# Performance work log

Hardware: AMD Instinct MI355X
Metric: run time of the kernel (lower is better)

## Reference

```python
import jax, jax.numpy as jnp
import numpy as np

B, H = 65536, 19


def _nbr(x):
    # 4-neighbor sum, equivalent to conv2d with cross kernel [[0,1,0],[1,0,1],[0,1,0]], padding=1
    p = jnp.pad(x, ((0, 0), (1, 1), (1, 1)))
    return p[:, :-2, 1:-1] + p[:, 2:, 1:-1] + p[:, 1:-1, :-2] + p[:, 1:-1, 2:]


def setup_inputs() -> dict:
    key = jax.random.key(0)
    k1, k2, k3 = jax.random.split(key, 3)
    # ternary board: 0 empty, 1 black, 2 white -> disjoint stone planes
    board = jax.random.randint(k1, (B, H, H), 0, 3)
    stones = jnp.stack([(board == 1), (board == 2)], axis=1).astype(jnp.float32)  # [B,2,H,H]
    current_player = jax.random.randint(k2, (B,), 0, 2, dtype=jnp.int32)
    ko_points = jax.random.randint(k3, (B, 2), 0, H, dtype=jnp.int32)  # all kos active (>=0)
    return {"stones": stones, "current_player": current_player, "ko_points": ko_points}


def reference(stones, current_player, ko_points):
    f32 = jnp.float32
    cp = current_player[:, None, None]  # [B,1,1]
    cur = jnp.where(cp == 0, stones[:, 0], stones[:, 1])  # [B,H,H] float 0/1
    opp = jnp.where(cp == 0, stones[:, 1], stones[:, 0])
    empty = 1.0 - stones[:, 0] - stones[:, 1]             # float 0/1 (planes disjoint)
    empty_b = empty > 0.5

    # legal_moves()
    legal = empty_b & (_nbr(empty) > 0)
    opp_lib = _nbr(opp)
    weak = (opp > 0.5) & (opp_lib == 1)
    adj_weak = _nbr(weak.astype(f32)) > 0
    legal = legal | (empty_b & adj_weak)
    ids = jnp.arange(stones.shape[0])
    has_ko = ko_points[:, 0] >= 0
    rr = jnp.clip(ko_points[:, 0], 0, H - 1)
    cc = jnp.clip(ko_points[:, 1], 0, H - 1)
    legal = legal.at[ids, rr, cc].set(jnp.where(has_ko, False, legal[ids, rr, cc]))

    cur_lib = _nbr(cur) * empty
    turn = jnp.broadcast_to(current_player.astype(f32)[:, None, None], (stones.shape[0], H, H))
    return jnp.stack([cur, opp, legal.astype(f32), cur_lib, turn], axis=1)  # [B,5,H,H]
```

## Files before the change

### kernel.cpp

```cpp
#include <hip/hip_runtime.h>

#define GO_H 19
#define GO_HP 21
#define NCELL (GO_H * GO_H)
#define NPAD  (GO_HP * GO_HP)

__global__ __launch_bounds__(256) void go_features_kernel(
    const float* __restrict__ stones,
    const int*   __restrict__ cur_player,
    const int*   __restrict__ ko,
    float*       __restrict__ out)
{
    __shared__ float cur_p[NPAD];
    __shared__ float opp_p[NPAD];
    __shared__ float emp_p[NPAD];
    __shared__ float weak_p[NPAD];

    const int b   = blockIdx.x;
    const int tid = threadIdx.x;
    const int cp  = cur_player[b];

    const long long ibase = (long long)b * (2 * NCELL);
    const long long obase = (long long)b * (5 * NCELL);

    for (int i = tid; i < NPAD; i += 256) {
        cur_p[i]  = 0.f;
        opp_p[i]  = 0.f;
        emp_p[i]  = 0.f;
        weak_p[i] = 0.f;
    }
    __syncthreads();

    #pragma unroll
    for (int k = 0; k < 2; ++k) {
        int c = tid + k * 256;
        if (c < NCELL) {
            float s0 = stones[ibase + c];
            float s1 = stones[ibase + NCELL + c];
            float cu = cp ? s1 : s0;
            float op = cp ? s0 : s1;
            float em = 1.0f - s0 - s1;
            int r = c / GO_H, col = c % GO_H;
            int pi = (r + 1) * GO_HP + (col + 1);
            cur_p[pi] = cu;
            opp_p[pi] = op;
            emp_p[pi] = em;
        }
    }
    __syncthreads();

    #pragma unroll
    for (int k = 0; k < 2; ++k) {
        int c = tid + k * 256;
        if (c < NCELL) {
            int r = c / GO_H, col = c % GO_H;
            int pi = (r + 1) * GO_HP + (col + 1);
            float opl = opp_p[pi - GO_HP] + opp_p[pi + GO_HP]
                      + opp_p[pi - 1]     + opp_p[pi + 1];
            weak_p[pi] = (opp_p[pi] > 0.5f && opl == 1.0f) ? 1.f : 0.f;
        }
    }
    __syncthreads();

    int kr = ko[2 * b], kc = ko[2 * b + 1];
    bool has_ko = (kr >= 0);
    int rr = min(max(kr, 0), GO_H - 1);
    int cc = min(max(kc, 0), GO_H - 1);
    int koc = rr * GO_H + cc;
    float turn = (float)cp;

    #pragma unroll
    for (int k = 0; k < 2; ++k) {
        int c = tid + k * 256;
        if (c < NCELL) {
            int r = c / GO_H, col = c % GO_H;
            int pi = (r + 1) * GO_HP + (col + 1);
            float em  = emp_p[pi];
            bool  emb = em > 0.5f;
            float ne = emp_p[pi - GO_HP] + emp_p[pi + GO_HP]
                     + emp_p[pi - 1]     + emp_p[pi + 1];
            float nw = weak_p[pi - GO_HP] + weak_p[pi + GO_HP]
                     + weak_p[pi - 1]     + weak_p[pi + 1];
            bool legal = emb && (ne > 0.f || nw > 0.f);
            if (has_ko && c == koc) legal = false;
            float nc = cur_p[pi - GO_HP] + cur_p[pi + GO_HP]
                     + cur_p[pi - 1]     + cur_p[pi + 1];

            out[obase + c]             = cur_p[pi];
            out[obase + NCELL + c]     = opp_p[pi];
            out[obase + 2 * NCELL + c] = legal ? 1.f : 0.f;
            out[obase + 3 * NCELL + c] = nc * em;
            out[obase + 4 * NCELL + c] = turn;
        }
    }
}

extern "C" void kernel_launch(void* const* d_in, const int* in_sizes, int n_in,
                              void* d_out, int out_size, void* d_ws, size_t ws_size,
                              hipStream_t stream) {
    const float* stones     = (const float*)d_in[0];
    const int*   cur_player = (const int*)d_in[1];
    const int*   ko         = (const int*)d_in[2];
    float*       out        = (float*)d_out;

    const int B = in_sizes[1];
    go_features_kernel<<<B, 256, 0, stream>>>(stones, cur_player, ko, out);
}
```

Before: 607.7 us.

## Process four boards per block with vectorized raw loads and masked stencils

Each block now handles four boards instead of one. It copies the raw stone planes into shared memory with float4 loads and computes the padding-free neighbour sums using boundary masks rather than zero-padded shared buffers. This removes the per-board padding initialisation and one barrier, and it raises thread utilisation from 361 of 512 slots to full 256-wide loops over 1444 cells. The launch assumes B is divisible by 4 and that the stone base address is 16-byte aligned. Per-cell index arithmetic grows from the div/mod and mask selects.

```diff
diff --git a/kernel.cpp b/kernel.cpp
--- a/kernel.cpp
+++ b/kernel.cpp
@@ -1,97 +1,118 @@
 #include <hip/hip_runtime.h>
 
 #define GO_H 19
-#define GO_HP 21
-#define NCELL (GO_H * GO_H)
-#define NPAD  (GO_HP * GO_HP)
+#define NCELL 361
+#define G 4
+#define NIN (G * 2 * NCELL)
+#define NC_G (G * NCELL)
 
 __global__ __launch_bounds__(256) void go_features_kernel(
     const float* __restrict__ stones,
     const int*   __restrict__ cur_player,
     const int*   __restrict__ ko,
-    float*       __restrict__ out)
+    float*       __restrict__ out,
+    int B)
 {
-    __shared__ float cur_p[NPAD];
-    __shared__ float opp_p[NPAD];
-    __shared__ float emp_p[NPAD];
-    __shared__ float weak_p[NPAD];
+    __shared__ float sarr[NIN];
+    __shared__ float weak_s[NC_G];
+    __shared__ int   cp_s[G];
+    __shared__ int   koc_s[G];
+    __shared__ int   opp_off_s[G];
 
-    const int b   = blockIdx.x;
     const int tid = threadIdx.x;
-    const int cp  = cur_player[b];
+    const int gb  = blockIdx.x * G;
 
-    const long long ibase = (long long)b * (2 * NCELL);
-    const long long obase = (long long)b * (5 * NCELL);
+    {
+        const float4* in4 = (const float4*)(stones + (size_t)gb * (2 * NCELL));
+        float4* s4 = (float4*)sarr;
+        #pragma unroll
+        for (int i = tid; i < NIN / 4; i += 256) s4[i] = in4[i];
+    }
 
-    for (int i = tid; i < NPAD; i += 256) {
-        cur_p[i]  = 0.f;
-        opp_p[i]  = 0.f;
-        emp_p[i]  = 0.f;
-        weak_p[i] = 0.f;
+    if (tid < G) {
+        int b  = gb + tid;
+        int cp = cur_player[b];
+        cp_s[tid] = cp;
+        opp_off_s[tid] = tid * (2 * NCELL) + (cp == 0 ? NCELL : 0);
+        int kr = ko[2 * b], kc = ko[2 * b + 1];
+        int rr = min(max(kr, 0), GO_H - 1);
+        int cc = min(max(kc, 0), GO_H - 1);
+        koc_s[tid] = (kr >= 0) ? (rr * GO_H + cc) : -1;
     }
     __syncthreads();
 
-    #pragma unroll
-    for (int k = 0; k < 2; ++k) {
-        int c = tid + k * 256;
-        if (c < NCELL) {
-            float s0 = stones[ibase + c];
-            float s1 = stones[ibase + NCELL + c];
-            float cu = cp ? s1 : s0;
-            float op = cp ? s0 : s1;
-            float em = 1.0f - s0 - s1;
-            int r = c / GO_H, col = c % GO_H;
-            int pi = (r + 1) * GO_HP + (col + 1);
-            cur_p[pi] = cu;
-            opp_p[pi] = op;
-            emp_p[pi] = em;
-        }
+    for (int i = tid; i < NC_G; i += 256) {
+        int g   = i / NCELL;
+        int c   = i - g * NCELL;
+        int r   = c / GO_H;
+        int col = c - r * GO_H;
+        int ob  = opp_off_s[g];
+
+        float mu = (r > 0)          ? 1.f : 0.f;
+        float md = (r < GO_H - 1)   ? 1.f : 0.f;
+        float ml = (col > 0)        ? 1.f : 0.f;
+        float mr = (col < GO_H - 1) ? 1.f : 0.f;
+        int iu = (r > 0)          ? c - GO_H : c;
+        int id = (r < GO_H - 1)   ? c + GO_H : c;
+        int il = (col > 0)        ? c - 1    : c;
+        int ir = (col < GO_H - 1) ? c + 1    : c;
+
+        float opl = sarr[ob + iu] * mu + sarr[ob + id] * md
+                  + sarr[ob + il] * ml + sarr[ob + ir] * mr;
+        float osf = sarr[ob + c];
+        weak_s[i] = (osf > 0.5f && opl == 1.0f) ? 1.f : 0.f;
     }
     __syncthreads();
 
-    #pragma unroll
-    for (int k = 0; k < 2; ++k) {
-        int c = tid + k * 256;
-        if (c < NCELL) {
-            int r = c / GO_H, col = c % GO_H;
-            int pi = (r + 1) * GO_HP + (col + 1);
-            float opl = opp_p[pi - GO_HP] + opp_p[pi + GO_HP]
-                      + opp_p[pi - 1]     + opp_p[pi + 1];
-            weak_p[pi] = (opp_p[pi] > 0.5f && opl == 1.0f) ? 1.f : 0.f;
+    for (int i = tid; i < NC_G; i += 256) {
+        int g   = i / NCELL;
+        int c   = i - g * NCELL;
+        int r   = c / GO_H;
+        int col = c - r * GO_H;
+        int base = g * (2 * NCELL);
+        int cp   = cp_s[g];
+        int wb   = g * NCELL;
+
+        float mu = (r > 0)          ? 1.f : 0.f;
+        float md = (r < GO_H - 1)   ? 1.f : 0.f;
+        float ml = (col > 0)        ? 1.f : 0.f;
+        float mr = (col < GO_H - 1) ? 1.f : 0.f;
+        int iu = (r > 0)          ? c - GO_H : c;
+        int id = (r < GO_H - 1)   ? c + GO_H : c;
+        int il = (col > 0)        ? c - 1    : c;
+        int ir = (col < GO_H - 1) ? c + 1    : c;
+
+        float s0 = sarr[base + c];
+        float s1 = sarr[base + NCELL + c];
+        float cu = cp ? s1 : s0;
+        float op = cp ? s0 : s1;
+        float em = 1.f - s0 - s1;
+
+        float ne = 0.f, ncur = 0.f;
+        {
+            float n0, n1;
+            n0 = sarr[base + iu]; n1 = sarr[base + NCELL + iu];
+            ne += (1.f - n0 - n1) * mu;  ncur += (cp ? n1 : n0) * mu;
+            n0 = sarr[base + id]; n1 = sarr[base + NCELL + id];
+            ne += (1.f - n0 - n1) * md;  ncur += (cp ? n1 : n0) * md;
+            n0 = sarr[base + il]; n1 = sarr[base + NCELL + il];
+            ne += (1.f - n0 - n1) * ml;  ncur += (cp ? n1 : n0) * ml;
+            n0 = sarr[base + ir]; n1 = sarr[base + NCELL + ir];
+            ne += (1.f - n0 - n1) * mr;  ncur += (cp ? n1 : n0) * mr;
         }
-    }
-    __syncthreads();
+        float nw = weak_s[wb + iu] * mu + weak_s[wb + id] * md
+                 + weak_s[wb + il] * ml + weak_s[wb + ir] * mr;
 
-    int kr = ko[2 * b], kc = ko[2 * b + 1];
-    bool has_ko = (kr >= 0);
-    int rr = min(max(kr, 0), GO_H - 1);
-    int cc = min(max(kc, 0), GO_H - 1);
-    int koc = rr * GO_H + cc;
-    float turn = (float)cp;
+        bool emb   = em > 0.5f;
+        bool legal = emb && (ne > 0.f || nw > 0.f);
+        if (c == koc_s[g]) legal = false;
 
-    #pragma unroll
-    for (int k = 0; k < 2; ++k) {
-        int c = tid + k * 256;
-        if (c < NCELL) {
-            int r = c / GO_H, col = c % GO_H;
-            int pi = (r + 1) * GO_HP + (col + 1);
-            float em  = emp_p[pi];
-            bool  emb = em > 0.5f;
-            float ne = emp_p[pi - GO_HP] + emp_p[pi + GO_HP]
-                     + emp_p[pi - 1]     + emp_p[pi + 1];
-            float nw = weak_p[pi - GO_HP] + weak_p[pi + GO_HP]
-                     + weak_p[pi - 1]     + weak_p[pi + 1];
-            bool legal = emb && (ne > 0.f || nw > 0.f);
-            if (has_ko && c == koc) legal = false;
-            float nc = cur_p[pi - GO_HP] + cur_p[pi + GO_HP]
-                     + cur_p[pi - 1]     + cur_p[pi + 1];
-
-            out[obase + c]             = cur_p[pi];
-            out[obase + NCELL + c]     = opp_p[pi];
-            out[obase + 2 * NCELL + c] = legal ? 1.f : 0.f;
-            out[obase + 3 * NCELL + c] = nc * em;
-            out[obase + 4 * NCELL + c] = turn;
-        }
+        size_t obase = (size_t)(gb + g) * (5 * NCELL);
+        out[obase + c]             = cu;
+        out[obase + NCELL + c]     = op;
+        out[obase + 2 * NCELL + c] = legal ? 1.f : 0.f;
+        out[obase + 3 * NCELL + c] = ncur * em;
+        out[obase + 4 * NCELL + c] = (float)cp;
     }
 }
 
@@ -104,5 +125,6 @@
     float*       out        = (float*)d_out;
 
     const int B = in_sizes[1];
-    go_features_kernel<<<B, 256, 0, stream>>>(stones, cur_player, ko, out);
+    const int nblocks = B / G;
+    go_features_kernel<<<nblocks, 256, 0, stream>>>(stones, cur_player, ko, out, B);
 }
```

Result: faster. 583.3 us (-4.0%).

## Process two boards per block with border-only zeroing and index LUT

Applied to the files above, without the earlier changes.

Each 256-thread block now handles two boards instead of one, so 722 cells are spread across three thread iterations and fewer lanes sit idle. Only the padding border of the shared tiles is zeroed, the zeroing pass and its barrier are dropped, and a shared lookup table stores the padded index so the later passes skip the divide and modulo. Player and ko data are staged in shared memory. The cost is more shared memory per block and fewer blocks, and B must be divisible by two.

```diff
diff --git a/kernel.cpp b/kernel.cpp
--- a/kernel.cpp
+++ b/kernel.cpp
@@ -1,9 +1,11 @@
 #include <hip/hip_runtime.h>
 
-#define GO_H 19
+#define GO_H  19
 #define GO_HP 21
-#define NCELL (GO_H * GO_H)
-#define NPAD  (GO_HP * GO_HP)
+#define NCELL 361
+#define NPAD  441
+#define G     2
+#define NC_G  (G * NCELL)
 
 __global__ __launch_bounds__(256) void go_features_kernel(
     const float* __restrict__ stones,
@@ -11,86 +13,104 @@
     const int*   __restrict__ ko,
     float*       __restrict__ out)
 {
-    __shared__ float cur_p[NPAD];
-    __shared__ float opp_p[NPAD];
-    __shared__ float emp_p[NPAD];
-    __shared__ float weak_p[NPAD];
+    __shared__ float cur_p[G][NPAD];
+    __shared__ float opp_p[G][NPAD];
+    __shared__ float emp_p[G][NPAD];
+    __shared__ float weak_p[G][NPAD];
+    __shared__ unsigned short lut[NCELL];
+    __shared__ int cp_s[G], koc_s[G];
 
-    const int b   = blockIdx.x;
     const int tid = threadIdx.x;
-    const int cp  = cur_player[b];
+    const int gb  = blockIdx.x * G;
 
-    const long long ibase = (long long)b * (2 * NCELL);
-    const long long obase = (long long)b * (5 * NCELL);
-
-    for (int i = tid; i < NPAD; i += 256) {
-        cur_p[i]  = 0.f;
-        opp_p[i]  = 0.f;
-        emp_p[i]  = 0.f;
-        weak_p[i] = 0.f;
-    }
-    __syncthreads();
 
     #pragma unroll
     for (int k = 0; k < 2; ++k) {
-        int c = tid + k * 256;
-        if (c < NCELL) {
-            float s0 = stones[ibase + c];
-            float s1 = stones[ibase + NCELL + c];
-            float cu = cp ? s1 : s0;
-            float op = cp ? s0 : s1;
-            float em = 1.0f - s0 - s1;
-            int r = c / GO_H, col = c % GO_H;
-            int pi = (r + 1) * GO_HP + (col + 1);
-            cur_p[pi] = cu;
-            opp_p[pi] = op;
-            emp_p[pi] = em;
+        int i = tid + k * 256;
+        if (i < NPAD) {
+            int r = i / GO_HP, col = i - r * GO_HP;
+            if (r == 0 || r == GO_HP - 1 || col == 0 || col == GO_HP - 1) {
+                #pragma unroll
+                for (int g = 0; g < G; ++g) {
+                    cur_p[g][i] = 0.f; opp_p[g][i] = 0.f;
+                    emp_p[g][i] = 0.f; weak_p[g][i] = 0.f;
+                }
+            } else {
+                lut[(r - 1) * GO_H + (col - 1)] = (unsigned short)i;
+            }
+        }
+    }
+
+    if (tid < G) {
+        int b = gb + tid;
+        cp_s[tid] = cur_player[b];
+        int kr = ko[2 * b], kc = ko[2 * b + 1];
+        int rr = min(max(kr, 0), GO_H - 1);
+        int cc = min(max(kc, 0), GO_H - 1);
+        koc_s[tid] = (kr >= 0) ? rr * GO_H + cc : -1;
+    }
+
+    {
+        int c = tid, g = 0;
+        #pragma unroll
+        for (int k = 0; k < 3; ++k) {
+            if (g < G) {
+                int   cp = cur_player[gb + g];
+                const float* bp = stones + (size_t)(gb + g) * (2 * NCELL);
+                float s0 = bp[c];
+                float s1 = bp[NCELL + c];
+                int r = c / GO_H, col = c - r * GO_H;
+                int pi = (r + 1) * GO_HP + col + 1;
+                cur_p[g][pi] = cp ? s1 : s0;
+                opp_p[g][pi] = cp ? s0 : s1;
+                emp_p[g][pi] = 1.f - s0 - s1;
+            }
+            c += 256; if (c >= NCELL) { c -= NCELL; ++g; }
         }
     }
     __syncthreads();
 
-    #pragma unroll
-    for (int k = 0; k < 2; ++k) {
-        int c = tid + k * 256;
-        if (c < NCELL) {
-            int r = c / GO_H, col = c % GO_H;
-            int pi = (r + 1) * GO_HP + (col + 1);
-            float opl = opp_p[pi - GO_HP] + opp_p[pi + GO_HP]
-                      + opp_p[pi - 1]     + opp_p[pi + 1];
-            weak_p[pi] = (opp_p[pi] > 0.5f && opl == 1.0f) ? 1.f : 0.f;
+    {
+        int c = tid, g = 0;
+        #pragma unroll
+        for (int k = 0; k < 3; ++k) {
+            if (g < G) {
+                int pi = lut[c];
+                float o = opp_p[g][pi];
+                float s = opp_p[g][pi - GO_HP] + opp_p[g][pi + GO_HP]
+                        + opp_p[g][pi - 1]     + opp_p[g][pi + 1];
+                weak_p[g][pi] = (o > 0.5f && s == 1.0f) ? 1.f : 0.f;
+            }
+            c += 256; if (c >= NCELL) { c -= NCELL; ++g; }
         }
     }
     __syncthreads();
 
-    int kr = ko[2 * b], kc = ko[2 * b + 1];
-    bool has_ko = (kr >= 0);
-    int rr = min(max(kr, 0), GO_H - 1);
-    int cc = min(max(kc, 0), GO_H - 1);
-    int koc = rr * GO_H + cc;
-    float turn = (float)cp;
+    {
+        int c = tid, g = 0;
+        #pragma unroll
+        for (int k = 0; k < 3; ++k) {
+            if (g < G) {
+                int pi = lut[c];
+                float em = emp_p[g][pi];
+                float ne = emp_p[g][pi - GO_HP] + emp_p[g][pi + GO_HP]
+                         + emp_p[g][pi - 1]     + emp_p[g][pi + 1];
+                float nc = cur_p[g][pi - GO_HP] + cur_p[g][pi + GO_HP]
+                         + cur_p[g][pi - 1]     + cur_p[g][pi + 1];
+                float nw = weak_p[g][pi - GO_HP] + weak_p[g][pi + GO_HP]
+                         + weak_p[g][pi - 1]     + weak_p[g][pi + 1];
 
-    #pragma unroll
-    for (int k = 0; k < 2; ++k) {
-        int c = tid + k * 256;
-        if (c < NCELL) {
-            int r = c / GO_H, col = c % GO_H;
-            int pi = (r + 1) * GO_HP + (col + 1);
-            float em  = emp_p[pi];
-            bool  emb = em > 0.5f;
-            float ne = emp_p[pi - GO_HP] + emp_p[pi + GO_HP]
-                     + emp_p[pi - 1]     + emp_p[pi + 1];
-            float nw = weak_p[pi - GO_HP] + weak_p[pi + GO_HP]
-                     + weak_p[pi - 1]     + weak_p[pi + 1];
-            bool legal = emb && (ne > 0.f || nw > 0.f);
-            if (has_ko && c == koc) legal = false;
-            float nc = cur_p[pi - GO_HP] + cur_p[pi + GO_HP]
-                     + cur_p[pi - 1]     + cur_p[pi + 1];
+                bool legal = (em > 0.5f) && (ne > 0.f || nw > 0.f);
+                if (c == koc_s[g]) legal = false;
 
-            out[obase + c]             = cur_p[pi];
-            out[obase + NCELL + c]     = opp_p[pi];
-            out[obase + 2 * NCELL + c] = legal ? 1.f : 0.f;
-            out[obase + 3 * NCELL + c] = nc * em;
-            out[obase + 4 * NCELL + c] = turn;
+                size_t ob = (size_t)(gb + g) * (5 * NCELL);
+                out[ob + c]             = cur_p[g][pi];
+                out[ob + NCELL + c]     = opp_p[g][pi];
+                out[ob + 2 * NCELL + c] = legal ? 1.f : 0.f;
+                out[ob + 3 * NCELL + c] = nc * em;
+                out[ob + 4 * NCELL + c] = (float)cp_s[g];
+            }
+            c += 256; if (c >= NCELL) { c -= NCELL; ++g; }
         }
     }
 }
@@ -104,5 +124,5 @@
     float*       out        = (float*)d_out;
 
     const int B = in_sizes[1];
-    go_features_kernel<<<B, 256, 0, stream>>>(stones, cur_player, ko, out);
+    go_features_kernel<<<B / G, 256, 0, stream>>>(stones, cur_player, ko, out);
 }
```

After: 587.9 us. 1.03x faster.
